# Performance work log

Measured on AMD Instinct MI355X. Metric: run time of the kernel, lower is better.

The kernel has to match this reference:

```python
import jax, jax.numpy as jnp
import numpy as np

THRESHOLD = 1.25
CURRENT_DECAY = 0.25
VOLTAGE_DECAY = 0.03
SPIKE_PROB = 0.2


def setup_inputs() -> dict:
    key = jax.random.key(0)
    k1, k2 = jax.random.split(key)
    B, N, T = 2048, 16, 1024
    # binary input spike trains [batch, neurons, time]
    spike = (jax.random.uniform(k1, (B, N, T)) < SPIKE_PROB).astype(jnp.float32)
    # Dense synapse weight [out, in], no bias (lava-dl Dense default)
    W = jax.random.normal(k2, (N, N), dtype=jnp.float32) / np.sqrt(N)
    return {"spike": spike, "W": W}


def _cuba_dense(spike, W):
    # synaptic current input per timestep: z[b,o,t]
    z = jnp.einsum('oi,bit->bot', W, spike)
    zt = jnp.moveaxis(z, -1, 0)  # [T, B, O] for scan over time

    def step(carry, x):
        c, v = carry
        c = c * (1.0 - CURRENT_DECAY) + x
        v = v * (1.0 - VOLTAGE_DECAY) + c
        s = (v >= THRESHOLD).astype(v.dtype)
        v = v * (1.0 - s)  # hard reset to zero on spike
        return (c, v), s

    zero = jnp.zeros_like(zt[0])
    _, s = jax.lax.scan(step, (zero, zero), zt)  # s: [T, B, O]
    return jnp.moveaxis(s, 0, -1)  # [B, O, T]


def reference(spike, W):
    y = _cuba_dense(spike, W)  # [B, O, T] binary spikes
    # log-cosh free energy: exp(sum_neurons log(2 cosh(y))) -> [B, T]
    return jnp.exp(jnp.sum(jnp.log(2.0 * jnp.cosh(y)), axis=1))
```

## Files before the change

### kernel.cpp

```cpp
#include <hip/hip_runtime.h>
#include <stdint.h>

#define T_STEPS 1024
#define NWORDS  256
#define NB      8
#define SCAN_BLOCK (NB * 16)

typedef float f32x4 __attribute__((ext_vector_type(4)));

__global__ __launch_bounds__(256) void k_maskify(const float* __restrict__ spike,
                                                 unsigned long long* __restrict__ masks,
                                                 const float* __restrict__ W,
                                                 double* __restrict__ tab,
                                                 int B) {
    const int b  = blockIdx.x;
    const int tc = threadIdx.x;
    if (b < B) {
        const float4* sp = reinterpret_cast<const float4*>(spike) + (size_t)b * (16 * NWORDS);
        unsigned int m0 = 0, m1 = 0, m2 = 0, m3 = 0;
#pragma unroll
        for (int i = 0; i < 16; ++i) {
            float4 v = sp[i * NWORDS + tc];
            m0 |= (v.x >= 0.5f) ? (1u << i) : 0u;
            m1 |= (v.y >= 0.5f) ? (1u << i) : 0u;
            m2 |= (v.z >= 0.5f) ? (1u << i) : 0u;
            m3 |= (v.w >= 0.5f) ? (1u << i) : 0u;
        }
        masks[(size_t)b * NWORDS + tc] =
            (unsigned long long)m0 | ((unsigned long long)m1 << 16) |
            ((unsigned long long)m2 << 32) | ((unsigned long long)m3 << 48);
    } else {
        const int o = tc & 15;
        double w[16];
#pragma unroll
        for (int j = 0; j < 16; ++j) w[j] = (double)W[o * 16 + j];
#pragma unroll
        for (int k = 0; k < 32; ++k) {
            const int e    = tc + k * 256;
            const int byte = (e >> 4) & 255;
            const int s    = k >> 4;
            double slo = 0.0, shi = 0.0;
#pragma unroll
            for (int j = 0; j < 4; ++j) slo += (byte & (1 << j))  ? w[8 * s + j]     : 0.0;
#pragma unroll
            for (int j = 0; j < 4; ++j) shi += (byte & (16 << j)) ? w[8 * s + 4 + j] : 0.0;
            tab[s * 4096 + byte * 16 + o] = slo + shi;
        }
    }
}

__global__ __launch_bounds__(SCAN_BLOCK, 1) void k_scan(const double* __restrict__ tab,
                                                        const unsigned long long* __restrict__ masks,
                                                        float* __restrict__ out) {
    const int tid = threadIdx.x;
    const int bb  = tid >> 4;
    const int o   = tid & 15;
    const int b   = blockIdx.x * NB + bb;

    const uint64_t tb     = (uint64_t)tab;
    const uint64_t mb     = (uint64_t)masks;
    const uint64_t ob_out = (uint64_t)out;
    const uint32_t ob0    = (uint32_t)(o * 8);
    const uint32_t ob1    = ob0 + 32768u;
    const uint32_t vb_m   = (uint32_t)(b * (NWORDS * 8));
    const uint32_t vb_out = (uint32_t)(b * (T_STEPS * 4));
    const int grp_sh      = tid & 48;
    const bool writer     = (o == 0);

    double c = 0.0, v = 0.0;

    double T0_0, T0_1, T0_2, T0_3, T0_4, T0_5, T0_6, T0_7;
    double T1_0, T1_1, T1_2, T1_3, T1_4, T1_5, T1_6, T1_7;
    double T2_0, T2_1, T2_2, T2_3, T2_4, T2_5, T2_6, T2_7;
    unsigned long long M0, M1, M2, q0, q1;

#define GLT(DST, VOFF) \
    asm volatile("global_load_dwordx2 %0, %1, %2" : "=v"(DST) : "v"(VOFF), "s"(tb) : "memory")
#define GLM(DST, IDX) do { int _mi = (IDX); if (_mi > 255) _mi = 255;                 \
    const uint32_t _vo = vb_m + ((uint32_t)_mi << 3);                                 \
    asm volatile("global_load_dwordx2 %0, %1, %2" : "=v"(DST) : "v"(_vo), "s"(mb) : "memory"); } while (0)
#define WAITV(N) asm volatile("s_waitcnt vmcnt(" #N ")" ::: "memory")
#define SBAR __builtin_amdgcn_sched_barrier(0)

#define TISSUE(P, MW) do {                                                            \
    const uint32_t _lo = (uint32_t)(MW), _hi = (uint32_t)((MW) >> 32);                \
    uint32_t _a;                                                                      \
    _a = ob0 + ((_lo & 255u) << 7);          GLT(P##_0, _a);                          \
    _a = ob1 + (((_lo >> 8) & 255u) << 7);   GLT(P##_1, _a);                          \
    _a = ob0 + (((_lo >> 16) & 255u) << 7);  GLT(P##_2, _a);                          \
    _a = ob1 + ((_lo >> 24) << 7);           GLT(P##_3, _a);                          \
    _a = ob0 + ((_hi & 255u) << 7);          GLT(P##_4, _a);                          \
    _a = ob1 + (((_hi >> 8) & 255u) << 7);   GLT(P##_5, _a);                          \
    _a = ob0 + (((_hi >> 16) & 255u) << 7);  GLT(P##_6, _a);                          \
    _a = ob1 + ((_hi >> 24) << 7);           GLT(P##_7, _a);                          \
} while (0)

#define ZSTEP(ZL, ZH, OWEL) do {                                                      \
    const double _z = (ZL) + (ZH);                                                    \
    c = fma(c, 0.75, _z);                                                             \
    v = fma(v, 0.97, c);                                                              \
    const bool _s = (v >= 1.25);                                                      \
    const unsigned long long _bal = __ballot(_s);                                     \
    v = _s ? 0.0 : v;                                                                 \
    const uint32_t _k = __popc((uint32_t)(_bal >> grp_sh) & 0xFFFFu);                 \
    OWEL = exp2f(fmaf((float)_k, 0.62581400f, 16.0f));                                \
} while (0)

#define COMPUTE(P, W) do {                                                            \
    f32x4 _ow;                                                                        \
    ZSTEP(P##_0, P##_1, _ow.x);                                                       \
    ZSTEP(P##_2, P##_3, _ow.y);                                                       \
    ZSTEP(P##_4, P##_5, _ow.z);                                                       \
    ZSTEP(P##_6, P##_7, _ow.w);                                                       \
    if (writer) {                                                                     \
        const uint32_t _vo = vb_out + ((uint32_t)(W) << 4);                           \
        asm volatile("global_store_dwordx4 %0, %1, %2"                                \
                     :: "v"(_vo), "v"(_ow), "s"(ob_out) : "memory");                  \
    }                                                                                 \
} while (0)

#define BODY(W, TU, TI, MU, MI) do {                                                  \
    GLM(MI, (W) + 4);                                                                 \
    WAITV(12); SBAR;                                                                  \
    TISSUE(TI, MU); SBAR;                                                             \
    COMPUTE(TU, W);                                                                   \
} while (0)

    asm volatile("s_waitcnt vmcnt(0) lgkmcnt(0)" ::: "memory");

    GLM(q0, 0); GLM(q1, 1); GLM(M2, 2); GLM(M0, 3);
    WAITV(2); SBAR;
    TISSUE(T0, q0);
    TISSUE(T1, q1); SBAR;

    GLM(M1, 4);
    WAITV(9); SBAR;
    TISSUE(T2, M2); SBAR;
    COMPUTE(T0, 0);

    GLM(M2, 5);
    WAITV(11); SBAR;
    TISSUE(T0, M0); SBAR;
    COMPUTE(T1, 1);

    for (int w = 2; w < 254; w += 3) {
        BODY(w,     T2, T1, M1, M0);
        BODY(w + 1, T0, T2, M2, M1);
        BODY(w + 2, T1, T0, M0, M2);
    }

    WAITV(11); SBAR;
    COMPUTE(T2, 254);
    WAITV(2); SBAR;
    COMPUTE(T0, 255);

#undef GLT
#undef GLM
#undef WAITV
#undef SBAR
#undef TISSUE
#undef ZSTEP
#undef COMPUTE
#undef BODY
}

__global__ __launch_bounds__(SCAN_BLOCK) void k_scan_fb(const float* __restrict__ W,
                                                        const float* __restrict__ spike,
                                                        float* __restrict__ out) {
    __shared__ double ztab[4][16][16];
    __shared__ unsigned long long mlds[NB][NWORDS];
    __shared__ float outtab[17];
    const int tid = threadIdx.x, bb = tid >> 4, o = tid & 15;
    for (int e = tid; e < 4 * 16 * 16; e += SCAN_BLOCK) {
        const int oo = e & 15, idx = (e >> 4) & 15, seg = e >> 8;
        double s = 0.0;
#pragma unroll
        for (int j = 0; j < 4; ++j)
            if (idx & (1 << j)) s += (double)W[oo * 16 + seg * 4 + j];
        ztab[seg][idx][oo] = s;
    }
    if (tid < 17) {
        const double ln2 = 0.69314718055994530941723212145818;
        const double l2c1 = log(2.0 * cosh(1.0));
        outtab[tid] = (float)exp((16.0 - (double)tid) * ln2 + (double)tid * l2c1);
    }
    {
        const int part = tid & 15;
        const float4* spb = reinterpret_cast<const float4*>(spike) +
                            (size_t)(blockIdx.x * NB + bb) * (16 * NWORDS);
        for (int w = 0; w < 16; ++w) {
            const int tc = part * 16 + w;
            unsigned int m0 = 0, m1 = 0, m2 = 0, m3 = 0;
#pragma unroll
            for (int i = 0; i < 16; ++i) {
                float4 v = spb[i * NWORDS + tc];
                m0 |= (v.x >= 0.5f) ? (1u << i) : 0u;
                m1 |= (v.y >= 0.5f) ? (1u << i) : 0u;
                m2 |= (v.z >= 0.5f) ? (1u << i) : 0u;
                m3 |= (v.w >= 0.5f) ? (1u << i) : 0u;
            }
            mlds[bb][tc] = (unsigned long long)m0 | ((unsigned long long)m1 << 16) |
                           ((unsigned long long)m2 << 32) | ((unsigned long long)m3 << 48);
        }
    }
    __syncthreads();
    double c = 0.0, v = 0.0;
    const int b = blockIdx.x * NB + bb;
    float* outp = out + (size_t)b * T_STEPS;
    const int grp_sh = tid & 48;
    const bool writer = (o == 0);
    for (int tg = 0; tg < NWORDS; ++tg) {
        const unsigned long long mw = mlds[bb][tg];
#pragma unroll
        for (int j = 0; j < 4; ++j) {
            const unsigned int m = (unsigned int)(mw >> (16 * j)) & 0xFFFFu;
            const double z = (ztab[0][m & 15][o] + ztab[1][(m >> 4) & 15][o]) +
                             (ztab[2][(m >> 8) & 15][o] + ztab[3][(m >> 12) & 15][o]);
            c = fma(c, 0.75, z);
            v = fma(v, 0.97, c);
            const bool s = (v >= 1.25);
            const unsigned long long bal = __ballot(s);
            v = s ? 0.0 : v;
            if (writer) outp[tg * 4 + j] = outtab[(int)__popcll((bal >> grp_sh) & 0xFFFFull)];
        }
    }
}

extern "C" void kernel_launch(void* const* d_in, const int* in_sizes, int n_in,
                              void* d_out, int out_size, void* d_ws, size_t ws_size,
                              hipStream_t stream) {
    const float* spike = (const float*)d_in[0];
    const float* W     = (const float*)d_in[1];
    float* out         = (float*)d_out;

    const int B = in_sizes[0] / (16 * T_STEPS);

    const size_t mask_bytes = (size_t)B * NWORDS * sizeof(unsigned long long);
    const size_t tab_bytes  = 2 * 256 * 16 * sizeof(double);

    if (ws_size >= mask_bytes + tab_bytes) {
        unsigned long long* masks = (unsigned long long*)d_ws;
        double* tab = (double*)((char*)d_ws + mask_bytes);
        k_maskify<<<B + 1, 256, 0, stream>>>(spike, masks, W, tab, B);
        k_scan<<<B / NB, SCAN_BLOCK, 0, stream>>>(tab, masks, out);
    } else {
        k_scan_fb<<<B / NB, SCAN_BLOCK, 0, stream>>>(W, spike, out);
    }
}
```

Before: 93.26 us.

## Deepen table-load pipeline from three to four register buffers

Restructures the scan kernel's software pipeline to keep four sets of gathered z-table values in flight instead of three, prefetching mask words six ahead. Each iteration now computes on a buffer and then refills that same buffer, which is meant to hide more of the global-load latency behind the serial recurrence. The cost is more VGPRs, which may lower occupancy, and the hand-counted vmcnt waits must stay correct.

```diff
diff --git a/kernel.cpp b/kernel.cpp
--- a/kernel.cpp
+++ b/kernel.cpp
@@ -72,7 +72,8 @@
     double T0_0, T0_1, T0_2, T0_3, T0_4, T0_5, T0_6, T0_7;
     double T1_0, T1_1, T1_2, T1_3, T1_4, T1_5, T1_6, T1_7;
     double T2_0, T2_1, T2_2, T2_3, T2_4, T2_5, T2_6, T2_7;
-    unsigned long long M0, M1, M2, q0, q1;
+    double T3_0, T3_1, T3_2, T3_3, T3_4, T3_5, T3_6, T3_7;
+    unsigned long long MA, MB, MC, MD, q0, q1;
 
 #define GLT(DST, VOFF) \
     asm volatile("global_load_dwordx2 %0, %1, %2" : "=v"(DST) : "v"(VOFF), "s"(tb) : "memory")
@@ -106,53 +107,50 @@
     OWEL = exp2f(fmaf((float)_k, 0.62581400f, 16.0f));                                \
 } while (0)
 
-#define COMPUTE(P, W) do {                                                            \
+#define COMPUTE(P, WD) do {                                                           \
     f32x4 _ow;                                                                        \
     ZSTEP(P##_0, P##_1, _ow.x);                                                       \
     ZSTEP(P##_2, P##_3, _ow.y);                                                       \
     ZSTEP(P##_4, P##_5, _ow.z);                                                       \
     ZSTEP(P##_6, P##_7, _ow.w);                                                       \
     if (writer) {                                                                     \
-        const uint32_t _vo = vb_out + ((uint32_t)(W) << 4);                           \
+        const uint32_t _vo = vb_out + ((uint32_t)(WD) << 4);                          \
         asm volatile("global_store_dwordx4 %0, %1, %2"                                \
                      :: "v"(_vo), "v"(_ow), "s"(ob_out) : "memory");                  \
     }                                                                                 \
 } while (0)
 
-#define BODY(W, TU, TI, MU, MI) do {                                                  \
-    GLM(MI, (W) + 4);                                                                 \
-    WAITV(12); SBAR;                                                                  \
-    TISSUE(TI, MU); SBAR;                                                             \
-    COMPUTE(TU, W);                                                                   \
+#define BODY(WD, P, MU, MI) do {                                                      \
+    GLM(MI, (WD) + 6);                                                                \
+    WAITV(20); SBAR;                                                                  \
+    COMPUTE(P, WD);                                                                   \
+    TISSUE(P, MU); SBAR;                                                              \
 } while (0)
 
     asm volatile("s_waitcnt vmcnt(0) lgkmcnt(0)" ::: "memory");
 
-    GLM(q0, 0); GLM(q1, 1); GLM(M2, 2); GLM(M0, 3);
+    GLM(q0, 0); GLM(q1, 1); GLM(MA, 2); GLM(MB, 3); GLM(MC, 4); GLM(MD, 5);
     WAITV(2); SBAR;
     TISSUE(T0, q0);
-    TISSUE(T1, q1); SBAR;
-
-    GLM(M1, 4);
-    WAITV(9); SBAR;
-    TISSUE(T2, M2); SBAR;
-    COMPUTE(T0, 0);
-
-    GLM(M2, 5);
-    WAITV(11); SBAR;
-    TISSUE(T0, M0); SBAR;
-    COMPUTE(T1, 1);
-
-    for (int w = 2; w < 254; w += 3) {
-        BODY(w,     T2, T1, M1, M0);
-        BODY(w + 1, T0, T2, M2, M1);
-        BODY(w + 2, T1, T0, M0, M2);
-    }
-
-    WAITV(11); SBAR;
+    TISSUE(T1, q1);
+    TISSUE(T2, MA);
+    TISSUE(T3, MB); SBAR;
+
+    for (int w = 0; w < 252; w += 4) {
+        BODY(w,     T0, MC, MA);
+        BODY(w + 1, T1, MD, MB);
+        BODY(w + 2, T2, MA, MC);
+        BODY(w + 3, T3, MB, MD);
+    }
+
+    COMPUTE(T0, 252);
+    WAITV(21); SBAR;
+    COMPUTE(T1, 253);
+    WAITV(12); SBAR;
     COMPUTE(T2, 254);
-    WAITV(2); SBAR;
-    COMPUTE(T0, 255);
+    WAITV(3); SBAR;
+    COMPUTE(T3, 255);
+    asm volatile("s_waitcnt vmcnt(0)" ::: "memory");
 
 #undef GLT
 #undef GLM
```

New measurement: 91.94 us. Within noise of the previous version (-1.4%).
